# Optimization experiments

Hardware: AMD Instinct MI355X
Metric: run time of the kernel (lower is better)

Reference implementation:

```python
import jax, jax.numpy as jnp
import numpy as np

T = 1024
V = 512
K_BINS = jnp.array([1, 2, 3, 4, 5, 6, 7, 8, 12, 16, 24, 32, 48, 64, 96, 128], dtype=jnp.int32)
SPLIT_T = T // 2                      # int(T * 0.5)
CW = max(4, T // 20)                  # crossfade width = 51
FADE_START = SPLIT_T - CW // 2        # 487
FADE_END = SPLIT_T + CW // 2          # 537


def _early_weight():
    t = jnp.arange(T, dtype=jnp.float32)
    fade = 1.0 - (t - FADE_START) / (FADE_END - FADE_START)
    ew = jnp.where(t < FADE_START, 1.0, jnp.where(t < FADE_END, fade, 0.0))
    return ew.reshape(1, T, 1)


def setup_inputs() -> dict:
    key = jax.random.key(0)
    k = jax.random.split(key, 5)
    B = 64
    return {
        "x": jax.random.normal(k[0], (B, T, V), dtype=jnp.float32),
        "g_early_real": jax.random.normal(k[1], (V, 16), dtype=jnp.float32) * 0.1,
        "g_early_imag": jax.random.normal(k[2], (V, 16), dtype=jnp.float32) * 0.1,
        "g_late_real": jax.random.normal(k[3], (V, 16), dtype=jnp.float32) * 0.1,
        "g_late_imag": jax.random.normal(k[4], (V, 16), dtype=jnp.float32) * 0.1,
    }


def reference(x, g_early_real, g_early_imag, g_late_real, g_late_imag):
    # x: [B, T, V] real. rfft along time.
    X = jnp.fft.rfft(x, n=T, axis=1)              # [B, F, V] complex, F = T//2+1
    xb = X[:, K_BINS, :]                          # [B, K, V]
    # complex gain (1 + gr + i*gi), broadcast [1, K, V]
    g_e = (g_early_real + 1j * g_early_imag).T[None, :, :]
    g_l = (g_late_real + 1j * g_late_imag).T[None, :, :]
    Y_e = X.at[:, K_BINS, :].set(xb * (1.0 + g_e))
    Y_l = X.at[:, K_BINS, :].set(xb * (1.0 + g_l))
    y_early = jnp.fft.irfft(Y_e, n=T, axis=1)     # [B, T, V]
    y_late = jnp.fft.irfft(Y_l, n=T, axis=1)
    ew = _early_weight()
    return ew * y_early + (1.0 - ew) * y_late
```

## Files before the change

kernel.cpp:

```cpp
#include <hip/hip_runtime.h>
#include <math.h>

#define T_LEN 1024
#define VV 512
#define BB 64
#define NB 16
#define ANG_STEP 0.006135923151542565f
#define FADE_S 487
#define FADE_E 537

typedef float v4f __attribute__((ext_vector_type(4)));

__device__ constexpr int KB[NB] = {1,2,3,4,5,6,7,8,12,16,24,32,48,64,96,128};
__device__ constexpr float SGN[NB] = {-1.f, 1.f, -1.f, 1.f, -1.f, 1.f, -1.f, 1.f,
                                       1.f, 1.f,  1.f, 1.f,  1.f, 1.f,  1.f, 1.f};

__global__ __launch_bounds__(512, 1) void k_fused(const float* __restrict__ x,
                                                  const float* __restrict__ ger,
                                                  const float* __restrict__ gei,
                                                  const float* __restrict__ glr,
                                                  const float* __restrict__ gli,
                                                  float* __restrict__ Hg,
                                                  float* __restrict__ out) {
    const int b   = blockIdx.x;
    const int vc  = blockIdx.y;
    const int tid = threadIdx.x;
    const int vt  = tid & 31;
    const int th  = tid >> 5;

    __shared__ __align__(16) float2 tab[512][NB];
    __shared__ __align__(16) float  HB[64 * 128];
    float* scr = (float*)tab;

    for (int i = tid; i < 512 * NB; i += 512) {
        int t = i >> 4, j = i & 15;
        int idx = (KB[j] * t) & (T_LEN - 1);
        float ss, cc; sincosf(ANG_STEP * (float)idx, &ss, &cc);
        tab[t][j] = make_float2(cc, ss);
    }
    __syncthreads();

    float ar[4][NB], ai[4][NB];
#pragma unroll
    for (int k = 0; k < 4; ++k)
#pragma unroll
        for (int j = 0; j < NB; ++j) { ar[k][j] = 0.f; ai[k][j] = 0.f; }

    const int tbase = th * 64;
    const int ttab  = tbase & 511;
    const float4* xrd = (const float4*)(x + ((size_t)b * T_LEN + tbase) * VV + vc * 128) + vt;

#define DFT_T(TT, AV)                                           \
    do {                                                        \
        _Pragma("unroll")                                       \
        for (int j = 0; j < NB; ++j) {                          \
            float2 cs = tab[ttab + (TT)][j];                    \
            ar[0][j] = fmaf((AV).x, cs.x, ar[0][j]);            \
            ai[0][j] = fmaf(-(AV).x, cs.y, ai[0][j]);           \
            ar[1][j] = fmaf((AV).y, cs.x, ar[1][j]);            \
            ai[1][j] = fmaf(-(AV).y, cs.y, ai[1][j]);           \
            ar[2][j] = fmaf((AV).z, cs.x, ar[2][j]);            \
            ai[2][j] = fmaf(-(AV).z, cs.y, ai[2][j]);           \
            ar[3][j] = fmaf((AV).w, cs.x, ar[3][j]);            \
            ai[3][j] = fmaf(-(AV).w, cs.y, ai[3][j]);           \
        }                                                       \
    } while (0)

    {
        float4 a0 = xrd[(size_t)0 * 128];
        float4 a1 = xrd[(size_t)1 * 128];
        float4 a2 = xrd[(size_t)2 * 128];
        float4 a3 = xrd[(size_t)3 * 128];
#pragma unroll 1
        for (int i = 0; i < 60; i += 4) {
            float4 b0 = xrd[(size_t)(i + 4) * 128];
            float4 b1 = xrd[(size_t)(i + 5) * 128];
            float4 b2 = xrd[(size_t)(i + 6) * 128];
            float4 b3 = xrd[(size_t)(i + 7) * 128];
            DFT_T(i + 0, a0); DFT_T(i + 1, a1); DFT_T(i + 2, a2); DFT_T(i + 3, a3);
            a0 = b0; a1 = b1; a2 = b2; a3 = b3;
        }
        DFT_T(60, a0); DFT_T(61, a1); DFT_T(62, a2); DFT_T(63, a3);
    }
#undef DFT_T

    if (th >= 8) {
#pragma unroll
        for (int k = 0; k < 4; ++k)
#pragma unroll
            for (int j = 0; j < NB; ++j) { ar[k][j] *= SGN[j]; ai[k][j] *= SGN[j]; }
    }

    __syncthreads();

    const float scale = 2.0f / (float)T_LEN;
#pragma unroll
    for (int r = 0; r < 4; ++r) {
        const int j0 = r * 4;
#pragma unroll
        for (int k = 0; k < 4; ++k) {
            const int v = vt * 4 + k;
            float4* w = (float4*)(scr + (size_t)(th * 128 + v) * 8);
            w[0] = make_float4(ar[k][j0 + 0], ar[k][j0 + 1], ar[k][j0 + 2], ar[k][j0 + 3]);
            w[1] = make_float4(ai[k][j0 + 0], ai[k][j0 + 1], ai[k][j0 + 2], ai[k][j0 + 3]);
        }
        __syncthreads();
        {
            const int v  = tid & 127;
            const int jj = tid >> 7;
            const int j  = j0 + jj;
            float Xre = 0.f, Xim = 0.f;
#pragma unroll
            for (int t2 = 0; t2 < 16; ++t2) {
                Xre += scr[(size_t)(t2 * 128 + v) * 8 + jj];
                Xim += scr[(size_t)(t2 * 128 + v) * 8 + 4 + jj];
            }
            const int vg = vc * 128 + v;
            float er = ger[vg * NB + j], ei = gei[vg * NB + j];
            float lr = glr[vg * NB + j], li = gli[vg * NB + j];
            float here  = (Xre * er - Xim * ei) * scale;
            float heimN = -(Xre * ei + Xim * er) * scale;
            float hlre  = (Xre * lr - Xim * li) * scale;
            float hlimN = -(Xre * li + Xim * lr) * scale;
            HB[j * 128 + v]        = here;
            HB[(16 + j) * 128 + v] = heimN;
            HB[(32 + j) * 128 + v] = hlre;
            HB[(48 + j) * 128 + v] = hlimN;
            float* hg = Hg + (size_t)b * 64 * VV + vg;
            hg[(size_t)j * VV]        = here;
            hg[(size_t)(16 + j) * VV] = heimN;
            hg[(size_t)(32 + j) * VV] = hlre;
            hg[(size_t)(48 + j) * VV] = hlimN;
        }
        __syncthreads();
    }

    for (int i = tid; i < 512 * NB; i += 512) {
        int t = i >> 4, j = i & 15;
        int idx = (KB[j] * t) & (T_LEN - 1);
        float ss, cc; sincosf(ANG_STEP * (float)idx, &ss, &cc);
        tab[t][j] = make_float2(cc, ss);
    }
    __syncthreads();

    float hr0[NB], hr1[NB], hr2[NB], hr3[NB];
    float hi0[NB], hi1[NB], hi2[NB], hi3[NB];
    const int qb = (th < 8) ? 0 : 32;
#pragma unroll
    for (int j = 0; j < NB; ++j) {
        const float4 a  = *(const float4*)&HB[(qb + j)      * 128 + vt * 4];
        const float4 bq = *(const float4*)&HB[(qb + 16 + j) * 128 + vt * 4];
        const float sg = (th >= 8) ? SGN[j] : 1.0f;
        hr0[j] = a.x * sg;  hr1[j] = a.y * sg;  hr2[j] = a.z * sg;  hr3[j] = a.w * sg;
        hi0[j] = bq.x * sg; hi1[j] = bq.y * sg; hi2[j] = bq.z * sg; hi3[j] = bq.w * sg;
    }

    v4f* ow = (v4f*)(out + ((size_t)b * T_LEN + tbase) * VV + vc * 128) + vt;

#define APPLY_T(TT, AV)                                               \
    do {                                                              \
        float s0 = 0.f, s1 = 0.f, s2 = 0.f, s3 = 0.f;                 \
        _Pragma("unroll")                                             \
        for (int j = 0; j < NB; ++j) {                                \
            float2 cs = tab[ttab + (TT)][j];                          \
            s0 = fmaf(hr0[j], cs.x, s0); s0 = fmaf(hi0[j], cs.y, s0); \
            s1 = fmaf(hr1[j], cs.x, s1); s1 = fmaf(hi1[j], cs.y, s1); \
            s2 = fmaf(hr2[j], cs.x, s2); s2 = fmaf(hi2[j], cs.y, s2); \
            s3 = fmaf(hr3[j], cs.x, s3); s3 = fmaf(hi3[j], cs.y, s3); \
        }                                                             \
        v4f ov; ov.x = (AV).x + s0; ov.y = (AV).y + s1;               \
        ov.z = (AV).z + s2; ov.w = (AV).w + s3;                       \
        __builtin_nontemporal_store(ov, &ow[(size_t)(TT) * 128]);     \
    } while (0)

    {
        float4 a0 = xrd[(size_t)0 * 128];
        float4 a1 = xrd[(size_t)1 * 128];
        float4 a2 = xrd[(size_t)2 * 128];
        float4 a3 = xrd[(size_t)3 * 128];
#pragma unroll 1
        for (int i = 0; i < 60; i += 4) {
            float4 b0 = xrd[(size_t)(i + 4) * 128];
            float4 b1 = xrd[(size_t)(i + 5) * 128];
            float4 b2 = xrd[(size_t)(i + 6) * 128];
            float4 b3 = xrd[(size_t)(i + 7) * 128];
            APPLY_T(i + 0, a0); APPLY_T(i + 1, a1); APPLY_T(i + 2, a2); APPLY_T(i + 3, a3);
            a0 = b0; a1 = b1; a2 = b2; a3 = b3;
        }
        APPLY_T(60, a0); APPLY_T(61, a1); APPLY_T(62, a2); APPLY_T(63, a3);
    }
#undef APPLY_T
}

__global__ __launch_bounds__(512) void k_fixup(const float* __restrict__ x,
                                               const float* __restrict__ H,
                                               float* __restrict__ out) {
    const int b   = blockIdx.x;
    const int tz  = blockIdx.y;
    const int tid = threadIdx.x;
    const int ts  = tz ? 512 : FADE_S;
    const int te  = tz ? FADE_E : 512;
    const int nt  = te - ts;

    __shared__ float2 tab[32][NB];
    for (int i = tid; i < nt * NB; i += 512) {
        int t = i >> 4, j = i & 15;
        int idx = (KB[j] * (ts + t)) & (T_LEN - 1);
        float ss, cc; sincosf(ANG_STEP * (float)idx, &ss, &cc);
        tab[t][j] = make_float2(cc, ss);
    }

    float er[NB], ei[NB], lr[NB], li[NB];
    const float* hp = H + (size_t)b * 64 * VV + tid;
#pragma unroll
    for (int j = 0; j < NB; ++j) {
        er[j] = hp[(size_t)j        * VV];
        ei[j] = hp[(size_t)(16 + j) * VV];
        lr[j] = hp[(size_t)(32 + j) * VV];
        li[j] = hp[(size_t)(48 + j) * VV];
    }
    __syncthreads();

    const float* xrd = x + ((size_t)b * T_LEN + ts) * VV + tid;
    float*       ow  = out + ((size_t)b * T_LEN + ts) * VV + tid;

    for (int t = 0; t < nt; ++t) {
        float av = xrd[(size_t)t * VV];
        const int tg = ts + t;
        float se = 0.f, sl = 0.f;
#pragma unroll
        for (int j = 0; j < NB; ++j) {
            float2 cs = tab[t][j];
            se = fmaf(er[j], cs.x, se); se = fmaf(ei[j], cs.y, se);
            sl = fmaf(lr[j], cs.x, sl); sl = fmaf(li[j], cs.y, sl);
        }
        float w = 1.0f - (float)(tg - FADE_S) * (1.0f / 50.0f);
        ow[(size_t)t * VV] = av + fmaf(w, se - sl, sl);
    }
}

extern "C" void kernel_launch(void* const* d_in, const int* in_sizes, int n_in,
                              void* d_out, int out_size, void* d_ws, size_t ws_size,
                              hipStream_t stream) {
    (void)in_sizes; (void)n_in; (void)out_size; (void)ws_size;
    const float* x   = (const float*)d_in[0];
    const float* ger = (const float*)d_in[1];
    const float* gei = (const float*)d_in[2];
    const float* glr = (const float*)d_in[3];
    const float* gli = (const float*)d_in[4];
    float* out = (float*)d_out;

    float* Hg = (float*)d_ws;

    k_fused<<<dim3(BB, 4), 512, 0, stream>>>(x, ger, gei, glr, gli, Hg, out);
    k_fixup<<<dim3(BB, 2), 512, 0, stream>>>(x, Hg, out);
}
```

Before: 119.9 us.

## Remap threads to wave-per-128-timesteps with float2 columns and shallower reduction

```diff
diff --git a/kernel.cpp b/kernel.cpp
--- a/kernel.cpp
+++ b/kernel.cpp
@@ -9,7 +9,7 @@
 #define FADE_S 487
 #define FADE_E 537
 
-typedef float v4f __attribute__((ext_vector_type(4)));
+typedef float v2f __attribute__((ext_vector_type(2)));
 
 __device__ constexpr int KB[NB] = {1,2,3,4,5,6,7,8,12,16,24,32,48,64,96,128};
 __device__ constexpr float SGN[NB] = {-1.f, 1.f, -1.f, 1.f, -1.f, 1.f, -1.f, 1.f,
@@ -22,14 +22,13 @@
                                                   const float* __restrict__ gli,
                                                   float* __restrict__ Hg,
                                                   float* __restrict__ out) {
-    const int b   = blockIdx.x;
-    const int vc  = blockIdx.y;
-    const int tid = threadIdx.x;
-    const int vt  = tid & 31;
-    const int th  = tid >> 5;
+    const int b    = blockIdx.x;
+    const int vc   = blockIdx.y;
+    const int tid  = threadIdx.x;
+    const int wave = tid >> 6;
+    const int lane = tid & 63;
 
     __shared__ __align__(16) float2 tab[512][NB];
-    __shared__ __align__(16) float  HB[64 * 128];
     float* scr = (float*)tab;
 
     for (int i = tid; i < 512 * NB; i += 512) {
@@ -40,102 +39,146 @@
     }
     __syncthreads();
 
-    float ar[4][NB], ai[4][NB];
-#pragma unroll
-    for (int k = 0; k < 4; ++k)
-#pragma unroll
-        for (int j = 0; j < NB; ++j) { ar[k][j] = 0.f; ai[k][j] = 0.f; }
-
-    const int tbase = th * 64;
-    const int ttab  = tbase & 511;
-    const float4* xrd = (const float4*)(x + ((size_t)b * T_LEN + tbase) * VV + vc * 128) + vt;
+    float ar0[NB], ai0[NB], ar1[NB], ai1[NB];
+#pragma unroll
+    for (int j = 0; j < NB; ++j) { ar0[j] = ai0[j] = ar1[j] = ai1[j] = 0.f; }
+
+    const int trow = wave * 128;
+    const int ttab = trow & 511;
+    const float2* xrd = (const float2*)(x + ((size_t)b * T_LEN + trow) * VV + vc * 128) + lane;
 
 #define DFT_T(TT, AV)                                           \
     do {                                                        \
         _Pragma("unroll")                                       \
         for (int j = 0; j < NB; ++j) {                          \
             float2 cs = tab[ttab + (TT)][j];                    \
-            ar[0][j] = fmaf((AV).x, cs.x, ar[0][j]);            \
-            ai[0][j] = fmaf(-(AV).x, cs.y, ai[0][j]);           \
-            ar[1][j] = fmaf((AV).y, cs.x, ar[1][j]);            \
-            ai[1][j] = fmaf(-(AV).y, cs.y, ai[1][j]);           \
-            ar[2][j] = fmaf((AV).z, cs.x, ar[2][j]);            \
-            ai[2][j] = fmaf(-(AV).z, cs.y, ai[2][j]);           \
-            ar[3][j] = fmaf((AV).w, cs.x, ar[3][j]);            \
-            ai[3][j] = fmaf(-(AV).w, cs.y, ai[3][j]);           \
+            ar0[j] = fmaf((AV).x, cs.x, ar0[j]);                \
+            ai0[j] = fmaf(-(AV).x, cs.y, ai0[j]);               \
+            ar1[j] = fmaf((AV).y, cs.x, ar1[j]);                \
+            ai1[j] = fmaf(-(AV).y, cs.y, ai1[j]);               \
         }                                                       \
     } while (0)
 
     {
-        float4 a0 = xrd[(size_t)0 * 128];
-        float4 a1 = xrd[(size_t)1 * 128];
-        float4 a2 = xrd[(size_t)2 * 128];
-        float4 a3 = xrd[(size_t)3 * 128];
+        float2 a0 = xrd[(size_t)0 * 256];
+        float2 a1 = xrd[(size_t)1 * 256];
+        float2 a2 = xrd[(size_t)2 * 256];
+        float2 a3 = xrd[(size_t)3 * 256];
+        float2 a4 = xrd[(size_t)4 * 256];
+        float2 a5 = xrd[(size_t)5 * 256];
+        float2 a6 = xrd[(size_t)6 * 256];
+        float2 a7 = xrd[(size_t)7 * 256];
 #pragma unroll 1
-        for (int i = 0; i < 60; i += 4) {
-            float4 b0 = xrd[(size_t)(i + 4) * 128];
-            float4 b1 = xrd[(size_t)(i + 5) * 128];
-            float4 b2 = xrd[(size_t)(i + 6) * 128];
-            float4 b3 = xrd[(size_t)(i + 7) * 128];
+        for (int i = 0; i < 120; i += 8) {
+            float2 b0 = xrd[(size_t)(i +  8) * 256];
+            float2 b1 = xrd[(size_t)(i +  9) * 256];
+            float2 b2 = xrd[(size_t)(i + 10) * 256];
+            float2 b3 = xrd[(size_t)(i + 11) * 256];
+            float2 b4 = xrd[(size_t)(i + 12) * 256];
+            float2 b5 = xrd[(size_t)(i + 13) * 256];
+            float2 b6 = xrd[(size_t)(i + 14) * 256];
+            float2 b7 = xrd[(size_t)(i + 15) * 256];
             DFT_T(i + 0, a0); DFT_T(i + 1, a1); DFT_T(i + 2, a2); DFT_T(i + 3, a3);
+            DFT_T(i + 4, a4); DFT_T(i + 5, a5); DFT_T(i + 6, a6); DFT_T(i + 7, a7);
             a0 = b0; a1 = b1; a2 = b2; a3 = b3;
-        }
-        DFT_T(60, a0); DFT_T(61, a1); DFT_T(62, a2); DFT_T(63, a3);
+            a4 = b4; a5 = b5; a6 = b6; a7 = b7;
+        }
+        DFT_T(120, a0); DFT_T(121, a1); DFT_T(122, a2); DFT_T(123, a3);
+        DFT_T(124, a4); DFT_T(125, a5); DFT_T(126, a6); DFT_T(127, a7);
     }
 #undef DFT_T
 
-    if (th >= 8) {
-#pragma unroll
-        for (int k = 0; k < 4; ++k)
-#pragma unroll
-            for (int j = 0; j < NB; ++j) { ar[k][j] *= SGN[j]; ai[k][j] *= SGN[j]; }
-    }
-
+    if (wave >= 4) {
+#pragma unroll
+        for (int j = 0; j < NB; ++j) {
+            ar0[j] *= SGN[j]; ai0[j] *= SGN[j];
+            ar1[j] *= SGN[j]; ai1[j] *= SGN[j];
+        }
+    }
+    __syncthreads();
+
+    const int v0 = lane * 2;
+    float Xre[4], Xim[4];
+
+    if (wave < 4) {
+#pragma unroll
+        for (int j = 0; j < NB; ++j) {
+            scr[((size_t)wave * 128 + v0)     * 17 + j] = ar0[j];
+            scr[((size_t)wave * 128 + v0 + 1) * 17 + j] = ar1[j];
+        }
+    }
+    __syncthreads();
+    if (wave >= 4) {
+        const int w2 = wave - 4;
+#pragma unroll
+        for (int j = 0; j < NB; ++j) {
+            scr[((size_t)w2 * 128 + v0)     * 17 + j] += ar0[j];
+            scr[((size_t)w2 * 128 + v0 + 1) * 17 + j] += ar1[j];
+        }
+    }
+    __syncthreads();
+#pragma unroll
+    for (int q = 0; q < 4; ++q) {
+        const int c = tid * 4 + q;
+        const int vq = c >> 4, jq = c & 15;
+        Xre[q] = scr[((size_t)0 * 128 + vq) * 17 + jq]
+               + scr[((size_t)1 * 128 + vq) * 17 + jq]
+               + scr[((size_t)2 * 128 + vq) * 17 + jq]
+               + scr[((size_t)3 * 128 + vq) * 17 + jq];
+    }
+    __syncthreads();
+
+    if (wave < 4) {
+#pragma unroll
+        for (int j = 0; j < NB; ++j) {
+            scr[((size_t)wave * 128 + v0)     * 17 + j] = ai0[j];
+            scr[((size_t)wave * 128 + v0 + 1) * 17 + j] = ai1[j];
+        }
+    }
+    __syncthreads();
+    if (wave >= 4) {
+        const int w2 = wave - 4;
+#pragma unroll
+        for (int j = 0; j < NB; ++j) {
+            scr[((size_t)w2 * 128 + v0)     * 17 + j] += ai0[j];
+            scr[((size_t)w2 * 128 + v0 + 1) * 17 + j] += ai1[j];
+        }
+    }
+    __syncthreads();
+#pragma unroll
+    for (int q = 0; q < 4; ++q) {
+        const int c = tid * 4 + q;
+        const int vq = c >> 4, jq = c & 15;
+        Xim[q] = scr[((size_t)0 * 128 + vq) * 17 + jq]
+               + scr[((size_t)1 * 128 + vq) * 17 + jq]
+               + scr[((size_t)2 * 128 + vq) * 17 + jq]
+               + scr[((size_t)3 * 128 + vq) * 17 + jq];
+    }
     __syncthreads();
 
     const float scale = 2.0f / (float)T_LEN;
-#pragma unroll
-    for (int r = 0; r < 4; ++r) {
-        const int j0 = r * 4;
-#pragma unroll
-        for (int k = 0; k < 4; ++k) {
-            const int v = vt * 4 + k;
-            float4* w = (float4*)(scr + (size_t)(th * 128 + v) * 8);
-            w[0] = make_float4(ar[k][j0 + 0], ar[k][j0 + 1], ar[k][j0 + 2], ar[k][j0 + 3]);
-            w[1] = make_float4(ai[k][j0 + 0], ai[k][j0 + 1], ai[k][j0 + 2], ai[k][j0 + 3]);
-        }
-        __syncthreads();
-        {
-            const int v  = tid & 127;
-            const int jj = tid >> 7;
-            const int j  = j0 + jj;
-            float Xre = 0.f, Xim = 0.f;
-#pragma unroll
-            for (int t2 = 0; t2 < 16; ++t2) {
-                Xre += scr[(size_t)(t2 * 128 + v) * 8 + jj];
-                Xim += scr[(size_t)(t2 * 128 + v) * 8 + 4 + jj];
-            }
-            const int vg = vc * 128 + v;
-            float er = ger[vg * NB + j], ei = gei[vg * NB + j];
-            float lr = glr[vg * NB + j], li = gli[vg * NB + j];
-            float here  = (Xre * er - Xim * ei) * scale;
-            float heimN = -(Xre * ei + Xim * er) * scale;
-            float hlre  = (Xre * lr - Xim * li) * scale;
-            float hlimN = -(Xre * li + Xim * lr) * scale;
-            HB[j * 128 + v]        = here;
-            HB[(16 + j) * 128 + v] = heimN;
-            HB[(32 + j) * 128 + v] = hlre;
-            HB[(48 + j) * 128 + v] = hlimN;
-            float* hg = Hg + (size_t)b * 64 * VV + vg;
-            hg[(size_t)j * VV]        = here;
-            hg[(size_t)(16 + j) * VV] = heimN;
-            hg[(size_t)(32 + j) * VV] = hlre;
-            hg[(size_t)(48 + j) * VV] = hlimN;
-        }
-        __syncthreads();
-    }
-
-    for (int i = tid; i < 512 * NB; i += 512) {
+    {
+        float* hg = Hg + (size_t)b * 64 * VV;
+#pragma unroll
+        for (int q = 0; q < 4; ++q) {
+            const int c = tid * 4 + q;
+            const int vq = c >> 4, jq = c & 15;
+            const int vg = vc * 128 + vq;
+            float er = ger[vg * NB + jq], ei = gei[vg * NB + jq];
+            float lr = glr[vg * NB + jq], li = gli[vg * NB + jq];
+            float here  = (Xre[q] * er - Xim[q] * ei) * scale;
+            float heimN = -(Xre[q] * ei + Xim[q] * er) * scale;
+            float hlre  = (Xre[q] * lr - Xim[q] * li) * scale;
+            float hlimN = -(Xre[q] * li + Xim[q] * lr) * scale;
+            hg[(size_t)jq * VV + vg]        = here;
+            hg[(size_t)(16 + jq) * VV + vg] = heimN;
+            hg[(size_t)(32 + jq) * VV + vg] = hlre;
+            hg[(size_t)(48 + jq) * VV + vg] = hlimN;
+        }
+    }
+
+    __syncthreads();
+    for (int i = tid; i < 273 * NB; i += 512) {
         int t = i >> 4, j = i & 15;
         int idx = (KB[j] * t) & (T_LEN - 1);
         float ss, cc; sincosf(ANG_STEP * (float)idx, &ss, &cc);
@@ -143,51 +186,61 @@
     }
     __syncthreads();
 
-    float hr0[NB], hr1[NB], hr2[NB], hr3[NB];
-    float hi0[NB], hi1[NB], hi2[NB], hi3[NB];
-    const int qb = (th < 8) ? 0 : 32;
-#pragma unroll
-    for (int j = 0; j < NB; ++j) {
-        const float4 a  = *(const float4*)&HB[(qb + j)      * 128 + vt * 4];
-        const float4 bq = *(const float4*)&HB[(qb + 16 + j) * 128 + vt * 4];
-        const float sg = (th >= 8) ? SGN[j] : 1.0f;
-        hr0[j] = a.x * sg;  hr1[j] = a.y * sg;  hr2[j] = a.z * sg;  hr3[j] = a.w * sg;
-        hi0[j] = bq.x * sg; hi1[j] = bq.y * sg; hi2[j] = bq.z * sg; hi3[j] = bq.w * sg;
-    }
-
-    v4f* ow = (v4f*)(out + ((size_t)b * T_LEN + tbase) * VV + vc * 128) + vt;
+    float hr0[NB], hi0[NB], hr1[NB], hi1[NB];
+    {
+        const int qb = (wave < 4) ? 0 : 32;
+        const float* hgr = Hg + (size_t)b * 64 * VV + vc * 128;
+#pragma unroll
+        for (int j = 0; j < NB; ++j) {
+            const float sg = (wave >= 4) ? SGN[j] : 1.0f;
+            hr0[j] = hgr[(size_t)(qb + j) * VV + v0]          * sg;
+            hr1[j] = hgr[(size_t)(qb + j) * VV + v0 + 1]      * sg;
+            hi0[j] = hgr[(size_t)(qb + 16 + j) * VV + v0]     * sg;
+            hi1[j] = hgr[(size_t)(qb + 16 + j) * VV + v0 + 1] * sg;
+        }
+    }
+
+    v2f* ow = (v2f*)(out + ((size_t)b * T_LEN + trow) * VV + vc * 128) + lane;
 
 #define APPLY_T(TT, AV)                                               \
     do {                                                              \
-        float s0 = 0.f, s1 = 0.f, s2 = 0.f, s3 = 0.f;                 \
+        float s0 = 0.f, s1 = 0.f;                                     \
         _Pragma("unroll")                                             \
         for (int j = 0; j < NB; ++j) {                                \
             float2 cs = tab[ttab + (TT)][j];                          \
             s0 = fmaf(hr0[j], cs.x, s0); s0 = fmaf(hi0[j], cs.y, s0); \
             s1 = fmaf(hr1[j], cs.x, s1); s1 = fmaf(hi1[j], cs.y, s1); \
-            s2 = fmaf(hr2[j], cs.x, s2); s2 = fmaf(hi2[j], cs.y, s2); \
-            s3 = fmaf(hr3[j], cs.x, s3); s3 = fmaf(hi3[j], cs.y, s3); \
         }                                                             \
-        v4f ov; ov.x = (AV).x + s0; ov.y = (AV).y + s1;               \
-        ov.z = (AV).z + s2; ov.w = (AV).w + s3;                       \
-        __builtin_nontemporal_store(ov, &ow[(size_t)(TT) * 128]);     \
+        v2f ov; ov.x = (AV).x + s0; ov.y = (AV).y + s1;               \
+        __builtin_nontemporal_store(ov, &ow[(size_t)(TT) * 256]);     \
     } while (0)
 
     {
-        float4 a0 = xrd[(size_t)0 * 128];
-        float4 a1 = xrd[(size_t)1 * 128];
-        float4 a2 = xrd[(size_t)2 * 128];
-        float4 a3 = xrd[(size_t)3 * 128];
+        float2 a0 = xrd[(size_t)0 * 256];
+        float2 a1 = xrd[(size_t)1 * 256];
+        float2 a2 = xrd[(size_t)2 * 256];
+        float2 a3 = xrd[(size_t)3 * 256];
+        float2 a4 = xrd[(size_t)4 * 256];
+        float2 a5 = xrd[(size_t)5 * 256];
+        float2 a6 = xrd[(size_t)6 * 256];
+        float2 a7 = xrd[(size_t)7 * 256];
 #pragma unroll 1
-        for (int i = 0; i < 60; i += 4) {
-            float4 b0 = xrd[(size_t)(i + 4) * 128];
-            float4 b1 = xrd[(size_t)(i + 5) * 128];
-            float4 b2 = xrd[(size_t)(i + 6) * 128];
-            float4 b3 = xrd[(size_t)(i + 7) * 128];
+        for (int i = 0; i < 120; i += 8) {
+            float2 b0 = xrd[(size_t)(i +  8) * 256];
+            float2 b1 = xrd[(size_t)(i +  9) * 256];
+            float2 b2 = xrd[(size_t)(i + 10) * 256];
+            float2 b3 = xrd[(size_t)(i + 11) * 256];
+            float2 b4 = xrd[(size_t)(i + 12) * 256];
+            float2 b5 = xrd[(size_t)(i + 13) * 256];
+            float2 b6 = xrd[(size_t)(i + 14) * 256];
+            float2 b7 = xrd[(size_t)(i + 15) * 256];
             APPLY_T(i + 0, a0); APPLY_T(i + 1, a1); APPLY_T(i + 2, a2); APPLY_T(i + 3, a3);
+            APPLY_T(i + 4, a4); APPLY_T(i + 5, a5); APPLY_T(i + 6, a6); APPLY_T(i + 7, a7);
             a0 = b0; a1 = b1; a2 = b2; a3 = b3;
-        }
-        APPLY_T(60, a0); APPLY_T(61, a1); APPLY_T(62, a2); APPLY_T(63, a3);
+            a4 = b4; a5 = b5; a6 = b6; a7 = b7;
+        }
+        APPLY_T(120, a0); APPLY_T(121, a1); APPLY_T(122, a2); APPLY_T(123, a3);
+        APPLY_T(124, a4); APPLY_T(125, a5); APPLY_T(126, a6); APPLY_T(127, a7);
     }
 #undef APPLY_T
 }
```

After: 114.6 us. -4.4%, faster.

## Compute partial DFT and inverse via split-bf16 MFMA matrix multiplies

Applied to the files above, without the earlier changes.

```diff
diff --git a/kernel.cpp b/kernel.cpp
--- a/kernel.cpp
+++ b/kernel.cpp
@@ -9,187 +9,162 @@
 #define FADE_S 487
 #define FADE_E 537
 
-typedef float v4f __attribute__((ext_vector_type(4)));
+typedef short sh8 __attribute__((ext_vector_type(8)));
+typedef float f4  __attribute__((ext_vector_type(4)));
 
 __device__ constexpr int KB[NB] = {1,2,3,4,5,6,7,8,12,16,24,32,48,64,96,128};
-__device__ constexpr float SGN[NB] = {-1.f, 1.f, -1.f, 1.f, -1.f, 1.f, -1.f, 1.f,
-                                       1.f, 1.f,  1.f, 1.f,  1.f, 1.f,  1.f, 1.f};
-
-__global__ __launch_bounds__(512, 1) void k_fused(const float* __restrict__ x,
-                                                  const float* __restrict__ ger,
-                                                  const float* __restrict__ gei,
-                                                  const float* __restrict__ glr,
-                                                  const float* __restrict__ gli,
-                                                  float* __restrict__ Hg,
-                                                  float* __restrict__ out) {
-    const int b   = blockIdx.x;
-    const int vc  = blockIdx.y;
-    const int tid = threadIdx.x;
-    const int vt  = tid & 31;
-    const int th  = tid >> 5;
-
-    __shared__ __align__(16) float2 tab[512][NB];
-    __shared__ __align__(16) float  HB[64 * 128];
-    float* scr = (float*)tab;
-
-    for (int i = tid; i < 512 * NB; i += 512) {
-        int t = i >> 4, j = i & 15;
-        int idx = (KB[j] * t) & (T_LEN - 1);
-        float ss, cc; sincosf(ANG_STEP * (float)idx, &ss, &cc);
-        tab[t][j] = make_float2(cc, ss);
-    }
-    __syncthreads();
-
-    float ar[4][NB], ai[4][NB];
-#pragma unroll
-    for (int k = 0; k < 4; ++k)
-#pragma unroll
-        for (int j = 0; j < NB; ++j) { ar[k][j] = 0.f; ai[k][j] = 0.f; }
-
-    const int tbase = th * 64;
-    const int ttab  = tbase & 511;
-    const float4* xrd = (const float4*)(x + ((size_t)b * T_LEN + tbase) * VV + vc * 128) + vt;
-
-#define DFT_T(TT, AV)                                           \
-    do {                                                        \
-        _Pragma("unroll")                                       \
-        for (int j = 0; j < NB; ++j) {                          \
-            float2 cs = tab[ttab + (TT)][j];                    \
-            ar[0][j] = fmaf((AV).x, cs.x, ar[0][j]);            \
-            ai[0][j] = fmaf(-(AV).x, cs.y, ai[0][j]);           \
-            ar[1][j] = fmaf((AV).y, cs.x, ar[1][j]);            \
-            ai[1][j] = fmaf(-(AV).y, cs.y, ai[1][j]);           \
-            ar[2][j] = fmaf((AV).z, cs.x, ar[2][j]);            \
-            ai[2][j] = fmaf(-(AV).z, cs.y, ai[2][j]);           \
-            ar[3][j] = fmaf((AV).w, cs.x, ar[3][j]);            \
-            ai[3][j] = fmaf(-(AV).w, cs.y, ai[3][j]);           \
-        }                                                       \
-    } while (0)
-
-    {
-        float4 a0 = xrd[(size_t)0 * 128];
-        float4 a1 = xrd[(size_t)1 * 128];
-        float4 a2 = xrd[(size_t)2 * 128];
-        float4 a3 = xrd[(size_t)3 * 128];
-#pragma unroll 1
-        for (int i = 0; i < 60; i += 4) {
-            float4 b0 = xrd[(size_t)(i + 4) * 128];
-            float4 b1 = xrd[(size_t)(i + 5) * 128];
-            float4 b2 = xrd[(size_t)(i + 6) * 128];
-            float4 b3 = xrd[(size_t)(i + 7) * 128];
-            DFT_T(i + 0, a0); DFT_T(i + 1, a1); DFT_T(i + 2, a2); DFT_T(i + 3, a3);
-            a0 = b0; a1 = b1; a2 = b2; a3 = b3;
-        }
-        DFT_T(60, a0); DFT_T(61, a1); DFT_T(62, a2); DFT_T(63, a3);
-    }
-#undef DFT_T
-
-    if (th >= 8) {
-#pragma unroll
-        for (int k = 0; k < 4; ++k)
-#pragma unroll
-            for (int j = 0; j < NB; ++j) { ar[k][j] *= SGN[j]; ai[k][j] *= SGN[j]; }
-    }
-
-    __syncthreads();
-
-    const float scale = 2.0f / (float)T_LEN;
-#pragma unroll
-    for (int r = 0; r < 4; ++r) {
-        const int j0 = r * 4;
-#pragma unroll
-        for (int k = 0; k < 4; ++k) {
-            const int v = vt * 4 + k;
-            float4* w = (float4*)(scr + (size_t)(th * 128 + v) * 8);
-            w[0] = make_float4(ar[k][j0 + 0], ar[k][j0 + 1], ar[k][j0 + 2], ar[k][j0 + 3]);
-            w[1] = make_float4(ai[k][j0 + 0], ai[k][j0 + 1], ai[k][j0 + 2], ai[k][j0 + 3]);
-        }
+
+__device__ inline unsigned short f2bf(float f) {
+    union { float f; unsigned u; } x; x.f = f;
+    unsigned u = x.u + 0x7FFF + ((x.u >> 16) & 1);
+    return (unsigned short)(u >> 16);
+}
+__device__ inline float bf2f(unsigned short h) {
+    union { unsigned u; float f; } x; x.u = ((unsigned)h) << 16; return x.f;
+}
+__device__ inline void store_split(unsigned short* hi, unsigned short* lo, int idx, float f) {
+    unsigned short h = f2bf(f);
+    hi[idx] = h;
+    lo[idx] = f2bf(f - bf2f(h));
+}
+
+__global__ __launch_bounds__(256) void k_tables(unsigned short* __restrict__ CS1hi,
+                                                unsigned short* __restrict__ CS1lo,
+                                                unsigned short* __restrict__ A2hi,
+                                                unsigned short* __restrict__ A2lo) {
+    int idx = blockIdx.x * 256 + threadIdx.x;
+    int q = idx & 31, t = idx >> 5;
+    int j = q >> 1;
+    int a = (KB[j] * t) & (T_LEN - 1);
+    float ss, cc; sincosf(ANG_STEP * (float)a, &ss, &cc);
+    float cs1 = (q & 1) ? -ss : cc;
+    float a2  = (q & 1) ?  ss : cc;
+    store_split(CS1hi, CS1lo, q * 1024 + t, cs1);
+    store_split(A2hi,  A2lo,  t * 32 + q,  a2);
+}
+
+__global__ __launch_bounds__(256, 2) void k_mfma(const float* __restrict__ x,
+                                                 const float* __restrict__ ger,
+                                                 const float* __restrict__ gei,
+                                                 const float* __restrict__ glr,
+                                                 const float* __restrict__ gli,
+                                                 const unsigned short* __restrict__ CS1hi,
+                                                 const unsigned short* __restrict__ CS1lo,
+                                                 const unsigned short* __restrict__ A2hi,
+                                                 const unsigned short* __restrict__ A2lo,
+                                                 float* __restrict__ Hg,
+                                                 float* __restrict__ out) {
+    const int b    = blockIdx.x;
+    const int vc   = blockIdx.y;
+    const int tid  = threadIdx.x;
+    const int wave = tid >> 6;
+    const int l    = tid & 63;
+    const int v0   = vc * 64;
+
+    __shared__ __align__(16) unsigned short xthi[64 * 40], xtlo[64 * 40];
+    __shared__ __align__(16) unsigned short Hehi[64 * 40], Helo[64 * 40];
+    __shared__ __align__(16) unsigned short Hlhi[64 * 40], Hllo[64 * 40];
+
+    const int vl = tid & 63;
+    const int tq = tid >> 6;
+    const int lr16 = l & 15;
+    const int kg   = l >> 4;
+    const int nrow = wave * 16 + lr16;
+    const int vglob = v0 + nrow;
+
+    f4 acc0 = {0.f, 0.f, 0.f, 0.f};
+    f4 acc1 = {0.f, 0.f, 0.f, 0.f};
+
+    for (int tb = 0; tb < 32; ++tb) {
         __syncthreads();
         {
-            const int v  = tid & 127;
-            const int jj = tid >> 7;
-            const int j  = j0 + jj;
-            float Xre = 0.f, Xim = 0.f;
-#pragma unroll
-            for (int t2 = 0; t2 < 16; ++t2) {
-                Xre += scr[(size_t)(t2 * 128 + v) * 8 + jj];
-                Xim += scr[(size_t)(t2 * 128 + v) * 8 + 4 + jj];
+            const float* xp = x + ((size_t)(b * T_LEN + tb * 32 + tq * 8)) * VV + v0 + vl;
+            float vals[8];
+#pragma unroll
+            for (int i = 0; i < 8; ++i) vals[i] = xp[(size_t)i * VV];
+            sh8 phi, plo;
+#pragma unroll
+            for (int i = 0; i < 8; ++i) {
+                unsigned short h = f2bf(vals[i]);
+                phi[i] = (short)h;
+                plo[i] = (short)f2bf(vals[i] - bf2f(h));
             }
-            const int vg = vc * 128 + v;
-            float er = ger[vg * NB + j], ei = gei[vg * NB + j];
-            float lr = glr[vg * NB + j], li = gli[vg * NB + j];
-            float here  = (Xre * er - Xim * ei) * scale;
-            float heimN = -(Xre * ei + Xim * er) * scale;
-            float hlre  = (Xre * lr - Xim * li) * scale;
-            float hlimN = -(Xre * li + Xim * lr) * scale;
-            HB[j * 128 + v]        = here;
-            HB[(16 + j) * 128 + v] = heimN;
-            HB[(32 + j) * 128 + v] = hlre;
-            HB[(48 + j) * 128 + v] = hlimN;
-            float* hg = Hg + (size_t)b * 64 * VV + vg;
-            hg[(size_t)j * VV]        = here;
-            hg[(size_t)(16 + j) * VV] = heimN;
-            hg[(size_t)(32 + j) * VV] = hlre;
-            hg[(size_t)(48 + j) * VV] = hlimN;
+            *(sh8*)&xthi[vl * 40 + tq * 8] = phi;
+            *(sh8*)&xtlo[vl * 40 + tq * 8] = plo;
         }
         __syncthreads();
-    }
-
-    for (int i = tid; i < 512 * NB; i += 512) {
-        int t = i >> 4, j = i & 15;
-        int idx = (KB[j] * t) & (T_LEN - 1);
-        float ss, cc; sincosf(ANG_STEP * (float)idx, &ss, &cc);
-        tab[t][j] = make_float2(cc, ss);
+
+        const int kb = tb * 32 + kg * 8;
+        sh8 aH0 = *(const sh8*)&CS1hi[(size_t)lr16 * 1024 + kb];
+        sh8 aH1 = *(const sh8*)&CS1hi[(size_t)(lr16 + 16) * 1024 + kb];
+        sh8 aL0 = *(const sh8*)&CS1lo[(size_t)lr16 * 1024 + kb];
+        sh8 aL1 = *(const sh8*)&CS1lo[(size_t)(lr16 + 16) * 1024 + kb];
+        sh8 bH  = *(const sh8*)&xthi[nrow * 40 + kg * 8];
+        sh8 bL  = *(const sh8*)&xtlo[nrow * 40 + kg * 8];
+
+        acc0 = __builtin_amdgcn_mfma_f32_16x16x32_bf16(aH0, bH, acc0, 0, 0, 0);
+        acc0 = __builtin_amdgcn_mfma_f32_16x16x32_bf16(aH0, bL, acc0, 0, 0, 0);
+        acc0 = __builtin_amdgcn_mfma_f32_16x16x32_bf16(aL0, bH, acc0, 0, 0, 0);
+        acc1 = __builtin_amdgcn_mfma_f32_16x16x32_bf16(aH1, bH, acc1, 0, 0, 0);
+        acc1 = __builtin_amdgcn_mfma_f32_16x16x32_bf16(aH1, bL, acc1, 0, 0, 0);
+        acc1 = __builtin_amdgcn_mfma_f32_16x16x32_bf16(aL1, bH, acc1, 0, 0, 0);
+    }
+
+    {
+        const float scale = 2.0f / (float)T_LEN;
+        float* hg = Hg + (size_t)b * 64 * VV;
+#pragma unroll
+        for (int m = 0; m < 2; ++m) {
+            f4 acc = m ? acc1 : acc0;
+#pragma unroll
+            for (int p = 0; p < 2; ++p) {
+                const int j  = (l >> 4) * 2 + p + 8 * m;
+                const float Xr = acc[2 * p];
+                const float Xi = acc[2 * p + 1];
+                float er = ger[vglob * NB + j], ei = gei[vglob * NB + j];
+                float lrg = glr[vglob * NB + j], lig = gli[vglob * NB + j];
+                float h2ec = scale * (Xr * er - Xi * ei);
+                float h2es = -scale * (Xr * ei + Xi * er);
+                float h2lc = scale * (Xr * lrg - Xi * lig);
+                float h2ls = -scale * (Xr * lig + Xi * lrg);
+                hg[(size_t)j * VV + vglob]        = h2ec;
+                hg[(size_t)(16 + j) * VV + vglob] = h2es;
+                hg[(size_t)(32 + j) * VV + vglob] = h2lc;
+                hg[(size_t)(48 + j) * VV + vglob] = h2ls;
+                const int q0 = 2 * j, q1 = 2 * j + 1;
+                store_split(Hehi, Helo, nrow * 40 + q0, h2ec);
+                store_split(Hehi, Helo, nrow * 40 + q1, h2es);
+                store_split(Hlhi, Hllo, nrow * 40 + q0, h2lc);
+                store_split(Hlhi, Hllo, nrow * 40 + q1, h2ls);
+            }
+        }
     }
     __syncthreads();
 
-    float hr0[NB], hr1[NB], hr2[NB], hr3[NB];
-    float hi0[NB], hi1[NB], hi2[NB], hi3[NB];
-    const int qb = (th < 8) ? 0 : 32;
-#pragma unroll
-    for (int j = 0; j < NB; ++j) {
-        const float4 a  = *(const float4*)&HB[(qb + j)      * 128 + vt * 4];
-        const float4 bq = *(const float4*)&HB[(qb + 16 + j) * 128 + vt * 4];
-        const float sg = (th >= 8) ? SGN[j] : 1.0f;
-        hr0[j] = a.x * sg;  hr1[j] = a.y * sg;  hr2[j] = a.z * sg;  hr3[j] = a.w * sg;
-        hi0[j] = bq.x * sg; hi1[j] = bq.y * sg; hi2[j] = bq.z * sg; hi3[j] = bq.w * sg;
-    }
-
-    v4f* ow = (v4f*)(out + ((size_t)b * T_LEN + tbase) * VV + vc * 128) + vt;
-
-#define APPLY_T(TT, AV)                                               \
-    do {                                                              \
-        float s0 = 0.f, s1 = 0.f, s2 = 0.f, s3 = 0.f;                 \
-        _Pragma("unroll")                                             \
-        for (int j = 0; j < NB; ++j) {                                \
-            float2 cs = tab[ttab + (TT)][j];                          \
-            s0 = fmaf(hr0[j], cs.x, s0); s0 = fmaf(hi0[j], cs.y, s0); \
-            s1 = fmaf(hr1[j], cs.x, s1); s1 = fmaf(hi1[j], cs.y, s1); \
-            s2 = fmaf(hr2[j], cs.x, s2); s2 = fmaf(hi2[j], cs.y, s2); \
-            s3 = fmaf(hr3[j], cs.x, s3); s3 = fmaf(hi3[j], cs.y, s3); \
-        }                                                             \
-        v4f ov; ov.x = (AV).x + s0; ov.y = (AV).y + s1;               \
-        ov.z = (AV).z + s2; ov.w = (AV).w + s3;                       \
-        __builtin_nontemporal_store(ov, &ow[(size_t)(TT) * 128]);     \
-    } while (0)
-
-    {
-        float4 a0 = xrd[(size_t)0 * 128];
-        float4 a1 = xrd[(size_t)1 * 128];
-        float4 a2 = xrd[(size_t)2 * 128];
-        float4 a3 = xrd[(size_t)3 * 128];
-#pragma unroll 1
-        for (int i = 0; i < 60; i += 4) {
-            float4 b0 = xrd[(size_t)(i + 4) * 128];
-            float4 b1 = xrd[(size_t)(i + 5) * 128];
-            float4 b2 = xrd[(size_t)(i + 6) * 128];
-            float4 b3 = xrd[(size_t)(i + 7) * 128];
-            APPLY_T(i + 0, a0); APPLY_T(i + 1, a1); APPLY_T(i + 2, a2); APPLY_T(i + 3, a3);
-            a0 = b0; a1 = b1; a2 = b2; a3 = b3;
-        }
-        APPLY_T(60, a0); APPLY_T(61, a1); APPLY_T(62, a2); APPLY_T(63, a3);
-    }
-#undef APPLY_T
+    sh8 BeH = *(const sh8*)&Hehi[nrow * 40 + kg * 8];
+    sh8 BeL = *(const sh8*)&Helo[nrow * 40 + kg * 8];
+    sh8 BlH = *(const sh8*)&Hlhi[nrow * 40 + kg * 8];
+    sh8 BlL = *(const sh8*)&Hllo[nrow * 40 + kg * 8];
+
+#pragma unroll 2
+    for (int mt = 0; mt < 64; ++mt) {
+        const int t0 = mt * 16;
+        sh8 a2H = *(const sh8*)&A2hi[(size_t)(t0 + lr16) * 32 + kg * 8];
+        sh8 a2L = *(const sh8*)&A2lo[(size_t)(t0 + lr16) * 32 + kg * 8];
+        sh8 bH = (mt < 32) ? BeH : BlH;
+        sh8 bL = (mt < 32) ? BeL : BlL;
+        f4 acc = {0.f, 0.f, 0.f, 0.f};
+        acc = __builtin_amdgcn_mfma_f32_16x16x32_bf16(a2H, bH, acc, 0, 0, 0);
+        acc = __builtin_amdgcn_mfma_f32_16x16x32_bf16(a2H, bL, acc, 0, 0, 0);
+        acc = __builtin_amdgcn_mfma_f32_16x16x32_bf16(a2L, bH, acc, 0, 0, 0);
+#pragma unroll
+        for (int reg = 0; reg < 4; ++reg) {
+            const int t = t0 + (l >> 4) * 4 + reg;
+            const size_t off = ((size_t)(b * T_LEN + t)) * VV + vglob;
+            float val = x[off] + acc[reg];
+            __builtin_nontemporal_store(val, &out[off]);
+        }
+    }
 }
 
 __global__ __launch_bounds__(512) void k_fixup(const float* __restrict__ x,
@@ -250,8 +225,14 @@
     const float* gli = (const float*)d_in[4];
     float* out = (float*)d_out;
 
-    float* Hg = (float*)d_ws;
-
-    k_fused<<<dim3(BB, 4), 512, 0, stream>>>(x, ger, gei, glr, gli, Hg, out);
+    unsigned short* CS1hi = (unsigned short*)d_ws;
+    unsigned short* CS1lo = CS1hi + 32 * 1024;
+    unsigned short* A2hi  = CS1lo + 32 * 1024;
+    unsigned short* A2lo  = A2hi + 32 * 1024;
+    float* Hg = (float*)(A2lo + 32 * 1024);
+
+    k_tables<<<dim3(128), 256, 0, stream>>>(CS1hi, CS1lo, A2hi, A2lo);
+    k_mfma<<<dim3(BB, 8), 256, 0, stream>>>(x, ger, gei, glr, gli,
+                                            CS1hi, CS1lo, A2hi, A2lo, Hg, out);
     k_fixup<<<dim3(BB, 2), 512, 0, stream>>>(x, Hg, out);
 }
```

Result: faster. 117.0 us (-2.4%).
